# Kernel tuning notes

Measured on AMD Instinct MI355X. Metric: run time of the kernel, lower is better.

Reference implementation:

```python
import jax, jax.numpy as jnp
import numpy as np

B = 16          # number of trees (batch)
H = 256         # hidden_size == feature_size
S = 16          # Tree.num_sem
C = 5           # max_child_num (complete C-ary tree)
L = 6           # tree depth: leaves at level L, internal levels 0..L-1
N_LEAF = C**L                     # 15625
N_INT = (C**L - 1) // (C - 1)     # 3906 internal nodes, level-l offset = (C^l-1)/(C-1)


def setup_inputs() -> dict:
    key = jax.random.key(0)
    ks = jax.random.split(key, 20)
    rn = lambda k, shp, s=0.05: jax.random.normal(k, shp, dtype=jnp.float32) * s
    return {
        "leaf_box": jax.random.normal(ks[0], (B, N_LEAF, 4), dtype=jnp.float32),
        "leaf_sem": jax.random.uniform(ks[1], (B, N_LEAF, S), dtype=jnp.float32),
        "internal_box": jax.random.normal(ks[2], (B, N_INT, 4), dtype=jnp.float32),
        "node_type": jax.random.randint(ks[3], (B, N_INT), 0, 3, dtype=jnp.int32),
        "eps": jax.random.normal(ks[4], (B, H), dtype=jnp.float32),
        "W_box": rn(ks[5], (4, H)), "b_box": jnp.zeros((H,), jnp.float32),
        "W_sem": rn(ks[6], (S, H)), "b_sem": jnp.zeros((H,), jnp.float32),
        "W_node": rn(ks[7], (3, C * H, H)), "b_node": jnp.zeros((3, H), jnp.float32),
        "W1": rn(ks[8], (H, H)), "b1": jnp.zeros((H,), jnp.float32),
        "Wmu": rn(ks[9], (H, H)), "bmu": jnp.zeros((H,), jnp.float32),
        "Wvar": rn(ks[10], (H, H)), "bvar": jnp.zeros((H,), jnp.float32),
    }


def reference(leaf_box, leaf_sem, internal_box, node_type, eps,
              W_box, b_box, W_sem, b_sem, W_node, b_node,
              W1, b1, Wmu, bmu, Wvar, bvar):
    box_enc = lambda b: jax.nn.relu(b @ W_box + b_box)
    # LeafEncoder: relu-box-encoding + relu-sem-encoding
    feats = box_enc(leaf_box) + jax.nn.relu(leaf_sem @ W_sem + b_sem)  # [B, N_LEAF, H]
    # Bottom-up over internal levels (static loop over L=6 levels)
    for l in range(L - 1, -1, -1):
        n = C ** l
        off = (C ** l - 1) // (C - 1)
        child = feats.reshape(B, n, C * H)  # children flattened per parent (child_exists==1)
        # Apply all 3 branch encoders (vertical/horizontal/stack), select by node label
        y_all = jnp.einsum('bnk,tkh->bnth', child, W_node) + b_node          # [B,n,3,H]
        sel = jax.nn.one_hot(node_type[:, off:off + n], 3, dtype=child.dtype)  # [B,n,3]
        y = jnp.einsum('bnth,bnt->bnh', y_all, sel)
        feats = jax.nn.relu(y) + box_enc(internal_box[:, off:off + n])
    root = feats[:, 0]  # [B, H]
    # Sampler (variational, probabilistic)
    enc = jax.nn.relu(root @ W1 + b1)
    mu = enc @ Wmu + bmu
    logvar = enc @ Wvar + bvar
    std = jnp.exp(0.5 * logvar)
    kld = 1.0 + logvar - mu ** 2 - jnp.exp(logvar)
    return jnp.concatenate([eps * std + mu, kld], axis=1)  # [B, 2H]
```

## Files before the change

### kernel.cpp

```cpp
#include <hip/hip_runtime.h>


#define B_ 16
#define H_ 256
#define NLEAF 15625
#define NINT 3906

typedef __bf16 bf16_t;
typedef bf16_t bf16x8 __attribute__((ext_vector_type(8)));
typedef bf16_t bf16x4 __attribute__((ext_vector_type(4)));
typedef float f32x4 __attribute__((ext_vector_type(4)));

__device__ __forceinline__ void gl2lds16(const bf16_t* g, bf16_t* l) {
  __builtin_amdgcn_global_load_lds((const __attribute__((address_space(1))) void*)g,
                                   (__attribute__((address_space(3))) void*)l,
                                   16, 0, 0);
}

__global__ __launch_bounds__(256) void prep_kernel(const float* __restrict__ W_node,
                                                   bf16_t* __restrict__ Wt,
                                                   int* __restrict__ counters) {
  if (blockIdx.x == 0 && threadIdx.x < 18) counters[threadIdx.x] = 0;
  const int t = blockIdx.x / 80;
  const int kc = blockIdx.x % 80;
  const int h = threadIdx.x;
  const float* srcp = W_node + (size_t)t * 1280 * 256 + h;
  bf16_t* dstp = Wt + ((size_t)(t * 256 + h)) * 1280;
#pragma unroll
  for (int k0 = kc * 16; k0 < kc * 16 + 16; k0 += 8) {
    bf16x8 v;
#pragma unroll
    for (int j = 0; j < 8; ++j) v[j] = (bf16_t)srcp[(size_t)(k0 + j) * 256];
    *(bf16x8*)(dstp + k0) = v;
  }
}

__global__ __launch_bounds__(256) void leaf_kernel(
    const float* __restrict__ leaf_box, const float* __restrict__ leaf_sem,
    const float* __restrict__ W_box, const float* __restrict__ b_box,
    const float* __restrict__ W_sem, const float* __restrict__ b_sem,
    bf16_t* __restrict__ f6) {
  const int lane = threadIdx.x & 63;
  const int wave = threadIdx.x >> 6;
  const int q = lane >> 4;
  const int c = lane & 15;
  const int hh = wave & 1;
  const int gw = wave >> 1;

  bf16x8 wsem[8], wbox[8];
#pragma unroll
  for (int T = 0; T < 8; ++T) {
    const int hb = (hh * 8 + T) * 16 + c;
    bf16x8 a;
#pragma unroll
    for (int j = 0; j < 8; ++j) a[j] = (bf16_t)0.f;
    if (q < 2) {
#pragma unroll
      for (int j = 0; j < 8; ++j) a[j] = (bf16_t)W_sem[(q * 8 + j) * H_ + hb];
    } else if (q == 2) {
      a[0] = (bf16_t)b_sem[hb];
    }
    wsem[T] = a;
    bf16x8 b;
#pragma unroll
    for (int j = 0; j < 8; ++j) b[j] = (bf16_t)0.f;
    if (q == 0) {
#pragma unroll
      for (int j = 0; j < 4; ++j) b[j] = (bf16_t)W_box[j * H_ + hb];
      b[4] = (bf16_t)b_box[hb];
    }
    wbox[T] = b;
  }

  const int NG = (B_ * NLEAF) / 16;
  const int gstride = gridDim.x * 2;
  for (int g = blockIdx.x * 2 + gw; g < NG; g += gstride) {
    const int row = g * 16 + c;
    bf16x8 xs, xb;
#pragma unroll
    for (int j = 0; j < 8; ++j) { xs[j] = (bf16_t)0.f; xb[j] = (bf16_t)0.f; }
    if (q < 2) {
      const float4* sp = (const float4*)(leaf_sem + (size_t)row * 16 + q * 8);
      float4 s0 = sp[0], s1 = sp[1];
      xs[0] = (bf16_t)s0.x; xs[1] = (bf16_t)s0.y; xs[2] = (bf16_t)s0.z; xs[3] = (bf16_t)s0.w;
      xs[4] = (bf16_t)s1.x; xs[5] = (bf16_t)s1.y; xs[6] = (bf16_t)s1.z; xs[7] = (bf16_t)s1.w;
    } else if (q == 2) {
      xs[0] = (bf16_t)1.0f;
    }
    if (q == 0) {
      float4 bx = *(const float4*)(leaf_box + (size_t)row * 4);
      xb[0] = (bf16_t)bx.x; xb[1] = (bf16_t)bx.y; xb[2] = (bf16_t)bx.z; xb[3] = (bf16_t)bx.w;
      xb[4] = (bf16_t)1.0f;
    }
    bf16_t* orow = f6 + (size_t)row * H_ + hh * 128 + q * 4;
#pragma unroll
    for (int T = 0; T < 8; ++T) {
      f32x4 z = {0.f, 0.f, 0.f, 0.f};
      f32x4 as = __builtin_amdgcn_mfma_f32_16x16x32_bf16(wsem[T], xs, z, 0, 0, 0);
      f32x4 ab = __builtin_amdgcn_mfma_f32_16x16x32_bf16(wbox[T], xb, z, 0, 0, 0);
      bf16x4 o;
#pragma unroll
      for (int r = 0; r < 4; ++r)
        o[r] = (bf16_t)(fmaxf(as[r], 0.f) + fmaxf(ab[r], 0.f));
      *(bf16x4*)(orow + T * 16) = o;
    }
  }
}

__global__ __launch_bounds__(256) void bucket_kernel(const int* __restrict__ node_type,
                                                     int* __restrict__ counters,
                                                     int2* __restrict__ buckets) {
  __shared__ int lcnt[18];
  __shared__ int lbase[18];
  const int tid = threadIdx.x;
  if (tid < 18) lcnt[tid] = 0;
  __syncthreads();

  int idx = blockIdx.x * 256 + tid;
  bool active = idx < B_ * NINT;
  int t = 0, key = 0, mypos = 0;
  int2 e;
  int base = 0, nl_cap = 0;
  if (active) {
    int b = idx / NINT;
    int j = idx - b * NINT;
    int l, off;
    if (j >= 781)      { l = 5; off = 781; }
    else if (j >= 156) { l = 4; off = 156; }
    else if (j >= 31)  { l = 3; off = 31; }
    else if (j >= 6)   { l = 2; off = 6; }
    else if (j >= 1)   { l = 1; off = 1; }
    else               { l = 0; off = 0; }
    const int n_tab[6]    = {1, 5, 25, 125, 625, 3125};
    const int nn_tab[6]   = {5, 25, 125, 625, 3125, 15625};
    const int base_tab[6] = {0, 48, 288, 1488, 7488, 37488};
    int n_l = n_tab[l], nn = nn_tab[l];
    t = node_type[idx];
    int i = j - off;
    e.x = b * n_l + i;
    e.y = b * nn + 5 * i;
    base = base_tab[l];
    nl_cap = B_ * n_l;
    key = l * 3 + t;
    mypos = atomicAdd(&lcnt[key], 1);
  }
  __syncthreads();
  if (tid < 18) {
    int c = lcnt[tid];
    lbase[tid] = c ? atomicAdd(&counters[tid], c) : 0;
  }
  __syncthreads();
  if (active) {
    buckets[base + t * nl_cap + lbase[key] + mypos] = e;
  }
}

__global__ __launch_bounds__(256) void level_kernel(
    const bf16_t* __restrict__ src, bf16_t* __restrict__ dst,
    const int2* __restrict__ bucket, const int* __restrict__ counters,
    const bf16_t* __restrict__ Wt, const float* __restrict__ b_node,
    const float* __restrict__ ibox, const float* __restrict__ W_box,
    const float* __restrict__ b_box, int n_l, int off_l, int cap) {
  const int t = blockIdx.y;
  const int cnt = counters[t];
  const int tile0 = blockIdx.x * 128;
  if (tile0 >= cnt) return;
  const int nblk = blockIdx.z;
  const int2* rd = bucket + (size_t)t * cap;

  __shared__ __align__(16) bf16_t Asm[3][128][32];
  __shared__ __align__(16) bf16_t Bsm[3][128][32];

  const int tid = threadIdx.x;
  const int lane = tid & 63;
  const int wave = tid >> 6;
  const int wm = wave & 1, wn = wave >> 1;
  const int quad = lane >> 4;
  const int l15 = lane & 15;

  const int r4 = lane >> 2;
  const int c4 = lane & 3;
  const int gch = c4 ^ ((r4 >> 1) & 3);
  const bf16_t* wsrc = Wt + ((size_t)t * 256 + nblk * 128) * 1280;
  const bf16_t* aptr[2];
  const bf16_t* bptr[2];
#pragma unroll
  for (int i = 0; i < 2; ++i) {
    int r = wave * 32 + i * 16 + r4;
    int ai = tile0 + r;
    if (ai >= cnt) ai = cnt - 1;
    aptr[i] = src + (size_t)rd[ai].y * H_ + gch * 8;
    bptr[i] = wsrc + (size_t)r * 1280 + gch * 8;
  }

  f32x4 acc[4][4];
#pragma unroll
  for (int i = 0; i < 4; ++i)
#pragma unroll
    for (int j = 0; j < 4; ++j) acc[i][j] = (f32x4){0.f, 0.f, 0.f, 0.f};

  const int pcs = (quad ^ ((l15 >> 1) & 3)) * 8;

#define STAGE(buf, ks)                                  \
  {                                                     \
    const int ko = (ks) * 32;                           \
    bf16_t* la = &Asm[buf][0][0] + wave * 1024;         \
    bf16_t* lb = &Bsm[buf][0][0] + wave * 1024;         \
    gl2lds16(aptr[0] + ko, la);                         \
    gl2lds16(aptr[1] + ko, la + 512);                   \
    gl2lds16(bptr[0] + ko, lb);                         \
    gl2lds16(bptr[1] + ko, lb + 512);                   \
  }

#define FRAGS_AND_MFMA(bufv)                                                  \
  {                                                                           \
    bf16x8 af[4], bfr[4];                                                     \
    _Pragma("unroll") for (int am = 0; am < 4; ++am)                          \
        af[am] = *(const bf16x8*)(&Asm[bufv][wm * 64 + am * 16 + l15][pcs]);  \
    _Pragma("unroll") for (int bn = 0; bn < 4; ++bn)                          \
        bfr[bn] = *(const bf16x8*)(&Bsm[bufv][wn * 64 + bn * 16 + l15][pcs]); \
    __builtin_amdgcn_s_setprio(1);                                            \
    _Pragma("unroll") for (int am = 0; am < 4; ++am)                          \
        _Pragma("unroll") for (int bn = 0; bn < 4; ++bn)                      \
            acc[am][bn] = __builtin_amdgcn_mfma_f32_16x16x32_bf16(            \
                af[am], bfr[bn], acc[am][bn], 0, 0, 0);                       \
    __builtin_amdgcn_s_setprio(0);                                            \
  }

  STAGE(0, 0)
  STAGE(1, 1)
  int buf = 0, nxb = 2;
  for (int ks = 0; ks < 38; ++ks) {
    asm volatile("s_waitcnt vmcnt(4)" ::: "memory");
    __builtin_amdgcn_s_barrier();
    {
      bf16x8 af[4], bfr[4];
#pragma unroll
      for (int am = 0; am < 4; ++am)
        af[am] = *(const bf16x8*)(&Asm[buf][wm * 64 + am * 16 + l15][pcs]);
#pragma unroll
      for (int bn = 0; bn < 4; ++bn)
        bfr[bn] = *(const bf16x8*)(&Bsm[buf][wn * 64 + bn * 16 + l15][pcs]);
      STAGE(nxb, ks + 2)
      __builtin_amdgcn_s_setprio(1);
#pragma unroll
      for (int am = 0; am < 4; ++am)
#pragma unroll
        for (int bn = 0; bn < 4; ++bn)
          acc[am][bn] = __builtin_amdgcn_mfma_f32_16x16x32_bf16(af[am], bfr[bn], acc[am][bn], 0, 0, 0);
      __builtin_amdgcn_s_setprio(0);
    }
    buf = (buf == 2) ? 0 : buf + 1;
    nxb = (nxb == 2) ? 0 : nxb + 1;
  }
  asm volatile("s_waitcnt vmcnt(4)" ::: "memory");
  __builtin_amdgcn_s_barrier();
  FRAGS_AND_MFMA(buf)
  buf = (buf == 2) ? 0 : buf + 1;
  asm volatile("s_waitcnt vmcnt(0)" ::: "memory");
  __builtin_amdgcn_s_barrier();
  FRAGS_AND_MFMA(buf)
#undef FRAGS_AND_MFMA
#undef STAGE

  float wbv[4][6];
#pragma unroll
  for (int bn = 0; bn < 4; ++bn) {
    int col = nblk * 128 + wn * 64 + bn * 16 + l15;
    wbv[bn][0] = W_box[col];
    wbv[bn][1] = W_box[H_ + col];
    wbv[bn][2] = W_box[2 * H_ + col];
    wbv[bn][3] = W_box[3 * H_ + col];
    wbv[bn][4] = b_box[col];
    wbv[bn][5] = b_node[t * H_ + col];
  }
#pragma unroll
  for (int am = 0; am < 4; ++am) {
    int orow[4]; float4 bxv[4]; bool valid[4];
#pragma unroll
    for (int r = 0; r < 4; ++r) {
      int gidx = tile0 + wm * 64 + am * 16 + quad * 4 + r;
      valid[r] = (gidx < cnt);
      int ic = valid[r] ? gidx : (cnt - 1);
      int orw = rd[ic].x;
      orow[r] = orw;
      int b = orw / n_l;
      int i = orw - b * n_l;
      bxv[r] = *(const float4*)(ibox + ((size_t)b * NINT + off_l + i) * 4);
    }
#pragma unroll
    for (int bn = 0; bn < 4; ++bn) {
      int col = nblk * 128 + wn * 64 + bn * 16 + l15;
#pragma unroll
      for (int r = 0; r < 4; ++r) {
        if (!valid[r]) continue;
        float y = fmaxf(acc[am][bn][r] + wbv[bn][5], 0.f);
        float be = fmaf(wbv[bn][0], bxv[r].x,
                   fmaf(wbv[bn][1], bxv[r].y,
                   fmaf(wbv[bn][2], bxv[r].z,
                   fmaf(wbv[bn][3], bxv[r].w, wbv[bn][4]))));
        be = fmaxf(be, 0.f);
        dst[(size_t)orow[r] * H_ + col] = (bf16_t)(y + be);
      }
    }
  }
}

__global__ __launch_bounds__(256) void head_kernel(
    const bf16_t* __restrict__ f0, const float* __restrict__ eps,
    const float* __restrict__ W1, const float* __restrict__ b1,
    const float* __restrict__ Wmu, const float* __restrict__ bmu,
    const float* __restrict__ Wvar, const float* __restrict__ bvar,
    float* __restrict__ out) {
  __shared__ float root[256];
  __shared__ float enc[256];
  int b = blockIdx.x, h = threadIdx.x;
  root[h] = (float)f0[b * H_ + h];
  __syncthreads();
  float a = b1[h];
  for (int k = 0; k < 256; ++k) a = fmaf(root[k], W1[k * H_ + h], a);
  enc[h] = fmaxf(a, 0.f);
  __syncthreads();
  float m = bmu[h], lv = bvar[h];
  for (int k = 0; k < 256; ++k) {
    float e = enc[k];
    m = fmaf(e, Wmu[k * H_ + h], m);
    lv = fmaf(e, Wvar[k * H_ + h], lv);
  }
  float stdv = expf(0.5f * lv);
  float kld = 1.f + lv - m * m - expf(lv);
  out[b * 512 + h] = eps[b * H_ + h] * stdv + m;
  out[b * 512 + 256 + h] = kld;
}

extern "C" void kernel_launch(void* const* d_in, const int* in_sizes, int n_in,
                              void* d_out, int out_size, void* d_ws, size_t ws_size,
                              hipStream_t stream) {
  const float* leaf_box     = (const float*)d_in[0];
  const float* leaf_sem     = (const float*)d_in[1];
  const float* internal_box = (const float*)d_in[2];
  const int*   node_type    = (const int*)d_in[3];
  const float* eps          = (const float*)d_in[4];
  const float* W_box        = (const float*)d_in[5];
  const float* b_box        = (const float*)d_in[6];
  const float* W_sem        = (const float*)d_in[7];
  const float* b_sem        = (const float*)d_in[8];
  const float* W_node       = (const float*)d_in[9];
  const float* b_node       = (const float*)d_in[10];
  const float* W1           = (const float*)d_in[11];
  const float* b1           = (const float*)d_in[12];
  const float* Wmu          = (const float*)d_in[13];
  const float* bmu          = (const float*)d_in[14];
  const float* Wvar         = (const float*)d_in[15];
  const float* bvar         = (const float*)d_in[16];
  float* out = (float*)d_out;

  char* p = (char*)d_ws;
  auto alloc = [&](size_t bytes) {
    char* r = p;
    p += (bytes + 255) & ~(size_t)255;
    return r;
  };
  bf16_t* Wt = (bf16_t*)alloc((size_t)3 * 256 * 1280 * 2);
  const int n_tab[7] = {1, 5, 25, 125, 625, 3125, 15625};
  bf16_t* f[7];
  for (int l = 0; l <= 6; ++l) f[l] = (bf16_t*)alloc((size_t)B_ * n_tab[l] * H_ * 2);
  int* counters = (int*)alloc(18 * 4);
  int2* buckets = (int2*)alloc((size_t)187488 * 8);

  hipLaunchKernelGGL(prep_kernel, dim3(240), dim3(256), 0, stream, W_node, Wt, counters);
  hipLaunchKernelGGL(leaf_kernel, dim3(1024), dim3(256), 0, stream,
                     leaf_box, leaf_sem, W_box, b_box, W_sem, b_sem, f[6]);
  hipLaunchKernelGGL(bucket_kernel, dim3((B_ * NINT + 255) / 256), dim3(256), 0, stream,
                     node_type, counters, buckets);

  const int lvl_base[6] = {0, 48, 288, 1488, 7488, 37488};
  const int off_tab[6]  = {0, 1, 6, 31, 156, 781};
  for (int l = 5; l >= 0; --l) {
    int cap = B_ * n_tab[l];
    int tiles = (cap + 127) / 128;
    hipLaunchKernelGGL(level_kernel, dim3(tiles, 3, 2), dim3(256), 0, stream,
                       f[l + 1], f[l], buckets + lvl_base[l], counters + l * 3,
                       Wt, b_node, internal_box, W_box, b_box,
                       n_tab[l], off_tab[l], cap);
  }
  hipLaunchKernelGGL(head_kernel, dim3(16), dim3(256), 0, stream,
                     f[0], eps, W1, b1, Wmu, bmu, Wvar, bvar, out);
}
```

Baseline: 381.4 us.

## Write child features pre-permuted in bucket order so level GEMM reads contiguous rows

Adds a dest_kernel that computes, for every node, its destination row in a type-sorted layout, so the leaf kernel and each level kernel scatter their outputs directly into the order the next level's GEMM consumes. Each parent's five children then sit in one contiguous 1280-element row per bucket position, and the A-operand loads no longer need an indirect bucket lookup. The cost moves to scattered writes on output and one extra small kernel plus an index buffer.

```diff
diff --git a/kernel.cpp b/kernel.cpp
--- a/kernel.cpp
+++ b/kernel.cpp
@@ -32,78 +32,6 @@
 #pragma unroll
     for (int j = 0; j < 8; ++j) v[j] = (bf16_t)srcp[(size_t)(k0 + j) * 256];
     *(bf16x8*)(dstp + k0) = v;
-  }
-}
-
-__global__ __launch_bounds__(256) void leaf_kernel(
-    const float* __restrict__ leaf_box, const float* __restrict__ leaf_sem,
-    const float* __restrict__ W_box, const float* __restrict__ b_box,
-    const float* __restrict__ W_sem, const float* __restrict__ b_sem,
-    bf16_t* __restrict__ f6) {
-  const int lane = threadIdx.x & 63;
-  const int wave = threadIdx.x >> 6;
-  const int q = lane >> 4;
-  const int c = lane & 15;
-  const int hh = wave & 1;
-  const int gw = wave >> 1;
-
-  bf16x8 wsem[8], wbox[8];
-#pragma unroll
-  for (int T = 0; T < 8; ++T) {
-    const int hb = (hh * 8 + T) * 16 + c;
-    bf16x8 a;
-#pragma unroll
-    for (int j = 0; j < 8; ++j) a[j] = (bf16_t)0.f;
-    if (q < 2) {
-#pragma unroll
-      for (int j = 0; j < 8; ++j) a[j] = (bf16_t)W_sem[(q * 8 + j) * H_ + hb];
-    } else if (q == 2) {
-      a[0] = (bf16_t)b_sem[hb];
-    }
-    wsem[T] = a;
-    bf16x8 b;
-#pragma unroll
-    for (int j = 0; j < 8; ++j) b[j] = (bf16_t)0.f;
-    if (q == 0) {
-#pragma unroll
-      for (int j = 0; j < 4; ++j) b[j] = (bf16_t)W_box[j * H_ + hb];
-      b[4] = (bf16_t)b_box[hb];
-    }
-    wbox[T] = b;
-  }
-
-  const int NG = (B_ * NLEAF) / 16;
-  const int gstride = gridDim.x * 2;
-  for (int g = blockIdx.x * 2 + gw; g < NG; g += gstride) {
-    const int row = g * 16 + c;
-    bf16x8 xs, xb;
-#pragma unroll
-    for (int j = 0; j < 8; ++j) { xs[j] = (bf16_t)0.f; xb[j] = (bf16_t)0.f; }
-    if (q < 2) {
-      const float4* sp = (const float4*)(leaf_sem + (size_t)row * 16 + q * 8);
-      float4 s0 = sp[0], s1 = sp[1];
-      xs[0] = (bf16_t)s0.x; xs[1] = (bf16_t)s0.y; xs[2] = (bf16_t)s0.z; xs[3] = (bf16_t)s0.w;
-      xs[4] = (bf16_t)s1.x; xs[5] = (bf16_t)s1.y; xs[6] = (bf16_t)s1.z; xs[7] = (bf16_t)s1.w;
-    } else if (q == 2) {
-      xs[0] = (bf16_t)1.0f;
-    }
-    if (q == 0) {
-      float4 bx = *(const float4*)(leaf_box + (size_t)row * 4);
-      xb[0] = (bf16_t)bx.x; xb[1] = (bf16_t)bx.y; xb[2] = (bf16_t)bx.z; xb[3] = (bf16_t)bx.w;
-      xb[4] = (bf16_t)1.0f;
-    }
-    bf16_t* orow = f6 + (size_t)row * H_ + hh * 128 + q * 4;
-#pragma unroll
-    for (int T = 0; T < 8; ++T) {
-      f32x4 z = {0.f, 0.f, 0.f, 0.f};
-      f32x4 as = __builtin_amdgcn_mfma_f32_16x16x32_bf16(wsem[T], xs, z, 0, 0, 0);
-      f32x4 ab = __builtin_amdgcn_mfma_f32_16x16x32_bf16(wbox[T], xb, z, 0, 0, 0);
-      bf16x4 o;
-#pragma unroll
-      for (int r = 0; r < 4; ++r)
-        o[r] = (bf16_t)(fmaxf(as[r], 0.f) + fmaxf(ab[r], 0.f));
-      *(bf16x4*)(orow + T * 16) = o;
-    }
   }
 }
 
@@ -155,16 +83,117 @@
   }
 }
 
+__global__ __launch_bounds__(256) void dest_kernel(const int2* __restrict__ buckets,
+                                                   const int* __restrict__ counters,
+                                                   int* __restrict__ wdest_all) {
+  int flat = blockIdx.x * 256 + threadIdx.x;
+  if (flat >= 187488) return;
+  int l, base, cap, coff;
+  if (flat >= 37488)      { l = 5; base = 37488; cap = 50000; coff = 62480; }
+  else if (flat >= 7488)  { l = 4; base = 7488;  cap = 10000; coff = 12480; }
+  else if (flat >= 1488)  { l = 3; base = 1488;  cap = 2000;  coff = 2480; }
+  else if (flat >= 288)   { l = 2; base = 288;   cap = 400;   coff = 480; }
+  else if (flat >= 48)    { l = 1; base = 48;    cap = 80;    coff = 80; }
+  else                    { l = 0; base = 0;     cap = 16;    coff = 0; }
+  int rel = flat - base;
+  int t = (rel >= 2 * cap) ? 2 : (rel >= cap ? 1 : 0);
+  int s = rel - t * cap;
+  const int* c3 = counters + l * 3;
+  int cnt = c3[t];
+  if (s >= cnt) return;
+  int pfx = (t > 0 ? c3[0] : 0) + (t > 1 ? c3[1] : 0);
+  int node = buckets[flat].x;
+  int grow = (pfx + s) * 5;
+  int* wp = wdest_all + coff + 5 * node;
+#pragma unroll
+  for (int c = 0; c < 5; ++c) wp[c] = grow + c;
+}
+
+__global__ __launch_bounds__(256) void leaf_kernel(
+    const float* __restrict__ leaf_box, const float* __restrict__ leaf_sem,
+    const float* __restrict__ W_box, const float* __restrict__ b_box,
+    const float* __restrict__ W_sem, const float* __restrict__ b_sem,
+    const int* __restrict__ wd6, bf16_t* __restrict__ f6) {
+  const int lane = threadIdx.x & 63;
+  const int wave = threadIdx.x >> 6;
+  const int q = lane >> 4;
+  const int c = lane & 15;
+  const int hh = wave & 1;
+  const int gw = wave >> 1;
+
+  bf16x8 wsem[8], wbox[8];
+#pragma unroll
+  for (int T = 0; T < 8; ++T) {
+    const int hb = (hh * 8 + T) * 16 + c;
+    bf16x8 a;
+#pragma unroll
+    for (int j = 0; j < 8; ++j) a[j] = (bf16_t)0.f;
+    if (q < 2) {
+#pragma unroll
+      for (int j = 0; j < 8; ++j) a[j] = (bf16_t)W_sem[(q * 8 + j) * H_ + hb];
+    } else if (q == 2) {
+      a[0] = (bf16_t)b_sem[hb];
+    }
+    wsem[T] = a;
+    bf16x8 b;
+#pragma unroll
+    for (int j = 0; j < 8; ++j) b[j] = (bf16_t)0.f;
+    if (q == 0) {
+#pragma unroll
+      for (int j = 0; j < 4; ++j) b[j] = (bf16_t)W_box[j * H_ + hb];
+      b[4] = (bf16_t)b_box[hb];
+    }
+    wbox[T] = b;
+  }
+
+  const int NG = (B_ * NLEAF) / 16;
+  const int gstride = gridDim.x * 2;
+  for (int g = blockIdx.x * 2 + gw; g < NG; g += gstride) {
+    const int row = g * 16 + c;
+    const int wd = wd6[row];
+    bf16x8 xs, xb;
+#pragma unroll
+    for (int j = 0; j < 8; ++j) { xs[j] = (bf16_t)0.f; xb[j] = (bf16_t)0.f; }
+    if (q < 2) {
+      const float4* sp = (const float4*)(leaf_sem + (size_t)row * 16 + q * 8);
+      float4 s0 = sp[0], s1 = sp[1];
+      xs[0] = (bf16_t)s0.x; xs[1] = (bf16_t)s0.y; xs[2] = (bf16_t)s0.z; xs[3] = (bf16_t)s0.w;
+      xs[4] = (bf16_t)s1.x; xs[5] = (bf16_t)s1.y; xs[6] = (bf16_t)s1.z; xs[7] = (bf16_t)s1.w;
+    } else if (q == 2) {
+      xs[0] = (bf16_t)1.0f;
+    }
+    if (q == 0) {
+      float4 bx = *(const float4*)(leaf_box + (size_t)row * 4);
+      xb[0] = (bf16_t)bx.x; xb[1] = (bf16_t)bx.y; xb[2] = (bf16_t)bx.z; xb[3] = (bf16_t)bx.w;
+      xb[4] = (bf16_t)1.0f;
+    }
+    bf16_t* orow = f6 + (size_t)wd * H_ + hh * 128 + q * 4;
+#pragma unroll
+    for (int T = 0; T < 8; ++T) {
+      f32x4 z = {0.f, 0.f, 0.f, 0.f};
+      f32x4 as = __builtin_amdgcn_mfma_f32_16x16x32_bf16(wsem[T], xs, z, 0, 0, 0);
+      f32x4 ab = __builtin_amdgcn_mfma_f32_16x16x32_bf16(wbox[T], xb, z, 0, 0, 0);
+      bf16x4 o;
+#pragma unroll
+      for (int r = 0; r < 4; ++r)
+        o[r] = (bf16_t)(fmaxf(as[r], 0.f) + fmaxf(ab[r], 0.f));
+      *(bf16x4*)(orow + T * 16) = o;
+    }
+  }
+}
+
 __global__ __launch_bounds__(256) void level_kernel(
     const bf16_t* __restrict__ src, bf16_t* __restrict__ dst,
     const int2* __restrict__ bucket, const int* __restrict__ counters,
     const bf16_t* __restrict__ Wt, const float* __restrict__ b_node,
     const float* __restrict__ ibox, const float* __restrict__ W_box,
-    const float* __restrict__ b_box, int n_l, int off_l, int cap) {
+    const float* __restrict__ b_box, const int* __restrict__ wdest,
+    int n_l, int off_l, int cap) {
   const int t = blockIdx.y;
   const int cnt = counters[t];
   const int tile0 = blockIdx.x * 128;
   if (tile0 >= cnt) return;
+  const int pfx = (t > 0 ? counters[0] : 0) + (t > 1 ? counters[1] : 0);
   const int nblk = blockIdx.z;
   const int2* rd = bucket + (size_t)t * cap;
 
@@ -182,14 +211,15 @@
   const int c4 = lane & 3;
   const int gch = c4 ^ ((r4 >> 1) & 3);
   const bf16_t* wsrc = Wt + ((size_t)t * 256 + nblk * 128) * 1280;
+  const bf16_t* asrc = src + (size_t)pfx * 1280;
   const bf16_t* aptr[2];
   const bf16_t* bptr[2];
 #pragma unroll
   for (int i = 0; i < 2; ++i) {
     int r = wave * 32 + i * 16 + r4;
-    int ai = tile0 + r;
-    if (ai >= cnt) ai = cnt - 1;
-    aptr[i] = src + (size_t)rd[ai].y * H_ + gch * 8;
+    int rowi = tile0 + r;
+    if (rowi >= cnt) rowi = cnt - 1;
+    aptr[i] = asrc + (size_t)rowi * 1280 + gch * 8;
     bptr[i] = wsrc + (size_t)r * 1280 + gch * 8;
   }
 
@@ -276,14 +306,14 @@
   }
 #pragma unroll
   for (int am = 0; am < 4; ++am) {
-    int orow[4]; float4 bxv[4]; bool valid[4];
+    size_t obase[4]; float4 bxv[4]; bool valid[4];
 #pragma unroll
     for (int r = 0; r < 4; ++r) {
       int gidx = tile0 + wm * 64 + am * 16 + quad * 4 + r;
       valid[r] = (gidx < cnt);
       int ic = valid[r] ? gidx : (cnt - 1);
       int orw = rd[ic].x;
-      orow[r] = orw;
+      obase[r] = (size_t)(wdest ? wdest[orw] : orw) * H_;
       int b = orw / n_l;
       int i = orw - b * n_l;
       bxv[r] = *(const float4*)(ibox + ((size_t)b * NINT + off_l + i) * 4);
@@ -300,7 +330,7 @@
                    fmaf(wbv[bn][2], bxv[r].z,
                    fmaf(wbv[bn][3], bxv[r].w, wbv[bn][4]))));
         be = fmaxf(be, 0.f);
-        dst[(size_t)orow[r] * H_ + col] = (bf16_t)(y + be);
+        dst[obase[r] + col] = (bf16_t)(y + be);
       }
     }
   }
@@ -367,21 +397,27 @@
   for (int l = 0; l <= 6; ++l) f[l] = (bf16_t*)alloc((size_t)B_ * n_tab[l] * H_ * 2);
   int* counters = (int*)alloc(18 * 4);
   int2* buckets = (int2*)alloc((size_t)187488 * 8);
+  int* wdest_all = (int*)alloc((size_t)312480 * 4);
 
   hipLaunchKernelGGL(prep_kernel, dim3(240), dim3(256), 0, stream, W_node, Wt, counters);
-  hipLaunchKernelGGL(leaf_kernel, dim3(1024), dim3(256), 0, stream,
-                     leaf_box, leaf_sem, W_box, b_box, W_sem, b_sem, f[6]);
   hipLaunchKernelGGL(bucket_kernel, dim3((B_ * NINT + 255) / 256), dim3(256), 0, stream,
                      node_type, counters, buckets);
+  hipLaunchKernelGGL(dest_kernel, dim3((187488 + 255) / 256), dim3(256), 0, stream,
+                     buckets, counters, wdest_all);
+  hipLaunchKernelGGL(leaf_kernel, dim3(1024), dim3(256), 0, stream,
+                     leaf_box, leaf_sem, W_box, b_box, W_sem, b_sem,
+                     wdest_all + 62480, f[6]);
 
   const int lvl_base[6] = {0, 48, 288, 1488, 7488, 37488};
   const int off_tab[6]  = {0, 1, 6, 31, 156, 781};
+  const int woff[6]     = {0, 0, 80, 480, 2480, 12480};
   for (int l = 5; l >= 0; --l) {
     int cap = B_ * n_tab[l];
     int tiles = (cap + 127) / 128;
+    const int* wdp = (l >= 1) ? (wdest_all + woff[l]) : nullptr;
     hipLaunchKernelGGL(level_kernel, dim3(tiles, 3, 2), dim3(256), 0, stream,
                        f[l + 1], f[l], buckets + lvl_base[l], counters + l * 3,
-                       Wt, b_node, internal_box, W_box, b_box,
+                       Wt, b_node, internal_box, W_box, b_box, wdp,
                        n_tab[l], off_tab[l], cap);
   }
   hipLaunchKernelGGL(head_kernel, dim3(16), dim3(256), 0, stream,
```

New measurement: 399.5 us. +4.8%, slower.
